# Optimization experiments

Measured on AMD Instinct MI355X. Metric: run time of the kernel, lower is better.

## Reference

```python
import jax, jax.numpy as jnp
import numpy as np

NEG = -1e32
EPS_LN = 1e-5

def _layer_norm(x, w, b):
    mu = jnp.mean(x, axis=-1, keepdims=True)
    var = jnp.mean((x - mu) ** 2, axis=-1, keepdims=True)
    return (x - mu) / jnp.sqrt(var + EPS_LN) * w + b

def setup_inputs() -> dict:
    key = jax.random.key(0)
    ks = jax.random.split(key, 10)
    B, S, D, H, F = 2, 2048, 1024, 16, 4096
    s = 0.02
    return {
        "query": jax.random.normal(ks[0], (B, S, D), jnp.float32),
        "key": jax.random.normal(ks[1], (B, S, D), jnp.float32),
        "values": jax.random.normal(ks[2], (B, S, D), jnp.float32),
        "Wk": jax.random.normal(ks[3], (D, D), jnp.float32) * s,
        "bk": jnp.zeros((D,), jnp.float32),
        "Wv": jax.random.normal(ks[4], (D, D), jnp.float32) * s,
        "bv": jnp.zeros((D,), jnp.float32),
        "Wo": jax.random.normal(ks[5], (D, D), jnp.float32) * s,
        "bo": jnp.zeros((D,), jnp.float32),
        "gammas": jax.random.normal(ks[6], (H, 1, 1), jnp.float32),
        "ln1_w": jnp.ones((D,), jnp.float32),
        "ln1_b": jnp.zeros((D,), jnp.float32),
        "W1": jax.random.normal(ks[7], (F, D), jnp.float32) * s,
        "b1": jnp.zeros((F,), jnp.float32),
        "W2": jax.random.normal(ks[8], (D, F), jnp.float32) * s,
        "b2": jnp.zeros((D,), jnp.float32),
        "ln2_w": jnp.ones((D,), jnp.float32),
        "ln2_b": jnp.zeros((D,), jnp.float32),
        "mask": 1,
    }

def _forward(query, key, values, Wk, bk, Wv, bv, Wo, bo, gammas,
             ln1_w, ln1_b, W1, b1, W2, b2, ln2_w, ln2_b, mask):
    B, S, D = query.shape
    H = gammas.shape[0]
    dk = D // H
    # kq_same=True: q and k both use k_linear
    def proj(x, W, b):
        return (x @ W.T + b).reshape(B, S, H, dk).transpose(0, 2, 1, 3)  # bhsd
    q = proj(query, Wk, bk)
    k = proj(key, Wk, bk)
    v = proj(values, Wv, bv)

    scores = jnp.einsum("bhqd,bhkd->bhqk", q, k) / np.sqrt(dk).astype(np.float32)
    # src_mask: np.triu(ones, k=mask)==0 -> allowed where j <= i + mask - 1
    allow = jnp.tril(jnp.ones((S, S), bool), k=mask - 1)[None, None]  # (1,1,S,S)

    # --- distance decay (no_grad block in torch) ---
    scores_ = jax.nn.softmax(jnp.where(allow, scores, NEG), axis=-1)
    scores_ = scores_ * allow.astype(scores_.dtype)
    distcum = jnp.cumsum(scores_, axis=-1)
    disttotal = jnp.sum(scores_, axis=-1, keepdims=True)
    idx = jnp.arange(S)
    position_effect = jnp.abs(idx[:, None] - idx[None, :]).astype(jnp.float32)[None, None]
    dist_scores = jnp.sqrt(jnp.clip((disttotal - distcum) * position_effect, 0.0, None))
    gamma = -jax.nn.softplus(gammas)[None]  # (1,H,1,1)
    total_effect = jnp.clip(jnp.exp(dist_scores * gamma), 1e-5, 1e5)
    total_effect = jax.lax.stop_gradient(total_effect)
    # ---

    scores = scores * total_effect
    scores = jnp.where(allow, scores, NEG)
    attn = jax.nn.softmax(scores, axis=-1)
    out = jnp.einsum("bhqk,bhkd->bhqd", attn, v)
    concat = out.transpose(0, 2, 1, 3).reshape(B, S, D)
    query2 = concat @ Wo.T + bo

    x = _layer_norm(query + query2, ln1_w, ln1_b)
    ff = jax.nn.relu(x @ W1.T + b1) @ W2.T + b2
    x = _layer_norm(x + ff, ln2_w, ln2_b)
    return x

def reference(query, key, values, Wk, bk, Wv, bv, Wo, bo, gammas,
              ln1_w, ln1_b, W1, b1, W2, b2, ln2_w, ln2_b, mask):
    return _forward(query, key, values, Wk, bk, Wv, bv, Wo, bo, gammas,
                    ln1_w, ln1_b, W1, b1, W2, b2, ln2_w, ln2_b, mask)
```

## Files before the change

kernel.cpp:

```cpp
#include <hip/hip_runtime.h>
#include <hip/hip_bf16.h>

#define B_   2
#define S_   2048
#define D_   1024
#define H_   16
#define DK_  64
#define F_   4096
#define M_   (B_*S_)
#define PD   72

typedef __attribute__((ext_vector_type(8))) short short8;
typedef __attribute__((ext_vector_type(4))) float f32x4;

__device__ __forceinline__ float bf2f(unsigned short s) { return __uint_as_float(((unsigned int)s) << 16); }
__device__ __forceinline__ unsigned short f2bf(float f) {
    unsigned int u = __float_as_uint(f);
    u += 0x7fffu + ((u >> 16) & 1u);
    return (unsigned short)(u >> 16);
}

__device__ __forceinline__ bool probe_f32(const unsigned int* p) {
    return *p == 0x3F800000u;
}
__device__ __forceinline__ float ld1e(const void* p, size_t idx, bool f32) {
    return f32 ? ((const float*)p)[idx] : bf2f(((const unsigned short*)p)[idx]);
}
__device__ __forceinline__ void st1e(void* p, size_t idx, bool f32, float v) {
    if (f32) ((float*)p)[idx] = v;
    else     ((unsigned short*)p)[idx] = f2bf(v);
}

__device__ __forceinline__ void async16(void* lds, const void* g) {
    __builtin_amdgcn_global_load_lds(
        (const __attribute__((address_space(1))) void*)g,
        (__attribute__((address_space(3))) void*)lds, 16, 0, 0);
}

__device__ __forceinline__ unsigned int cvt_pk_bf16(float a, float b) {
    unsigned int r;
    asm("v_cvt_pk_bf16_f32 %0, %1, %2" : "=v"(r) : "v"(a), "v"(b));
    return r;
}

template <bool IS_MAX>
__device__ __forceinline__ float block_reduce(float val, float* buf, int tid) {
    buf[tid] = val;
    __syncthreads();
    #pragma unroll
    for (int off = 128; off > 0; off >>= 1) {
        if (tid < off) {
            float o = buf[tid + off];
            buf[tid] = IS_MAX ? fmaxf(buf[tid], o) : (buf[tid] + o);
        }
        __syncthreads();
    }
    float r = buf[0];
    __syncthreads();
    return r;
}

__global__ __launch_bounds__(256) void cvt_all(
    const void* __restrict__ W1, const void* __restrict__ W2,
    const void* __restrict__ Wk, const void* __restrict__ Wv,
    const void* __restrict__ Wo,
    const void* __restrict__ Qi, const void* __restrict__ Ki,
    const void* __restrict__ Vi,
    unsigned short* __restrict__ W1b, unsigned short* __restrict__ W2b,
    unsigned short* __restrict__ Wkb, unsigned short* __restrict__ Wvb,
    unsigned short* __restrict__ Wob,
    unsigned short* __restrict__ qcb, unsigned short* __restrict__ kcb,
    unsigned short* __restrict__ vcb,
    const unsigned int* __restrict__ probe)
{
    const bool p32 = probe_f32(probe);
    const int blk = blockIdx.x;
    const void* src;
    unsigned short* dst;
    int off;
    if (blk < 2048)      { src = W1; dst = W1b; off = blk; }
    else if (blk < 4096) { src = W2; dst = W2b; off = blk - 2048; }
    else if (blk < 4608) { src = Wk; dst = Wkb; off = blk - 4096; }
    else if (blk < 5120) { src = Wv; dst = Wvb; off = blk - 4608; }
    else if (blk < 5632) { src = Wo; dst = Wob; off = blk - 5120; }
    else if (blk < 7680) { if (!p32) return; src = Qi; dst = qcb; off = blk - 5632; }
    else if (blk < 9728) { if (!p32) return; src = Ki; dst = kcb; off = blk - 7680; }
    else                 { if (!p32) return; src = Vi; dst = vcb; off = blk - 9728; }
    const int i8 = (off * 256 + threadIdx.x) * 8;
    if (p32) {
        const float4 a = *(const float4*)((const float*)src + i8);
        const float4 b = *(const float4*)((const float*)src + i8 + 4);
        short8 o;
        o[0] = (short)f2bf(a.x); o[1] = (short)f2bf(a.y);
        o[2] = (short)f2bf(a.z); o[3] = (short)f2bf(a.w);
        o[4] = (short)f2bf(b.x); o[5] = (short)f2bf(b.y);
        o[6] = (short)f2bf(b.z); o[7] = (short)f2bf(b.w);
        *(short8*)(dst + i8) = o;
    } else {
        *(uint4*)(dst + i8) = *(const uint4*)((const unsigned short*)src + i8);
    }
}

template <int RELU, int AEXT, int CEXT>
__device__ __forceinline__ void gemm_body(
    const void* __restrict__ A,
    const unsigned short* __restrict__ W,
    const void* __restrict__ bias,
    void* __restrict__ C,
    int M, int N, int K, bool p32, int bx, int by)
{
    __shared__ unsigned short As[2][128 * 32];
    __shared__ unsigned short Ws[2][128 * 32];

    const bool a32 = AEXT && p32;
    const bool c32 = CEXT && p32;

    const int tid = threadIdx.x;
    const int lane = tid & 63;
    const int w = tid >> 6;
    const int wr = w >> 1;
    const int wc = w & 1;
    const int col16 = lane & 15;
    const int quad = lane >> 4;

    const int m0 = by * 128;
    const int n0 = bx * 128;

    const int c0 = tid, c1 = 256 + tid;
    const int r0 = c0 >> 2, kc0 = (((c0 & 3) ^ ((c0 >> 3) & 3)) * 8);
    const int r1 = c1 >> 2, kc1 = (((c1 & 3) ^ ((c1 >> 3) & 3)) * 8);

    const int fcol = ((quad ^ ((col16 >> 1) & 3)) * 8);

    f32x4 acc[4][4];
    #pragma unroll
    for (int mt = 0; mt < 4; mt++)
        #pragma unroll
        for (int nt = 0; nt < 4; nt++)
            acc[mt][nt] = (f32x4){0.f, 0.f, 0.f, 0.f};

    auto stage = [&](int bb, int k0) {
        async16(&Ws[bb][c0 * 8], W + (size_t)(n0 + r0) * K + k0 + kc0);
        async16(&Ws[bb][c1 * 8], W + (size_t)(n0 + r1) * K + k0 + kc1);
        if (a32) {
            const float* a0 = (const float*)A + (size_t)(m0 + r0) * K + k0 + kc0;
            const float* a1 = (const float*)A + (size_t)(m0 + r1) * K + k0 + kc1;
            const float4 x0 = *(const float4*)a0, y0 = *(const float4*)(a0 + 4);
            const float4 x1 = *(const float4*)a1, y1 = *(const float4*)(a1 + 4);
            short8 s0, s1;
            s0[0] = (short)f2bf(x0.x); s0[1] = (short)f2bf(x0.y);
            s0[2] = (short)f2bf(x0.z); s0[3] = (short)f2bf(x0.w);
            s0[4] = (short)f2bf(y0.x); s0[5] = (short)f2bf(y0.y);
            s0[6] = (short)f2bf(y0.z); s0[7] = (short)f2bf(y0.w);
            s1[0] = (short)f2bf(x1.x); s1[1] = (short)f2bf(x1.y);
            s1[2] = (short)f2bf(x1.z); s1[3] = (short)f2bf(x1.w);
            s1[4] = (short)f2bf(y1.x); s1[5] = (short)f2bf(y1.y);
            s1[6] = (short)f2bf(y1.z); s1[7] = (short)f2bf(y1.w);
            *(short8*)&As[bb][c0 * 8] = s0;
            *(short8*)&As[bb][c1 * 8] = s1;
        } else {
            const unsigned short* Ab = (const unsigned short*)A;
            async16(&As[bb][c0 * 8], Ab + (size_t)(m0 + r0) * K + k0 + kc0);
            async16(&As[bb][c1 * 8], Ab + (size_t)(m0 + r1) * K + k0 + kc1);
        }
    };

    stage(0, 0);
    __syncthreads();
    int cur = 0;
    for (int k0 = 0; k0 < K; k0 += 32) {
        const int nxt = cur ^ 1;
        if (k0 + 32 < K) stage(nxt, k0 + 32);

        short8 av[4], bv[4];
        #pragma unroll
        for (int mt = 0; mt < 4; mt++)
            av[mt] = *(const short8*)&As[cur][(wr * 64 + mt * 16 + col16) * 32 + fcol];
        #pragma unroll
        for (int nt = 0; nt < 4; nt++)
            bv[nt] = *(const short8*)&Ws[cur][(wc * 64 + nt * 16 + col16) * 32 + fcol];
        #pragma unroll
        for (int mt = 0; mt < 4; mt++)
            #pragma unroll
            for (int nt = 0; nt < 4; nt++)
                acc[mt][nt] = __builtin_amdgcn_mfma_f32_16x16x32_bf16(
                    av[mt], bv[nt], acc[mt][nt], 0, 0, 0);
        __syncthreads();
        cur = nxt;
    }

    #pragma unroll
    for (int mt = 0; mt < 4; mt++) {
        const int row = m0 + wr * 64 + mt * 16 + quad * 4;
        #pragma unroll
        for (int nt = 0; nt < 4; nt++) {
            const int col = n0 + wc * 64 + nt * 16 + col16;
            const float bb = ld1e(bias, col, p32);
            #pragma unroll
            for (int r = 0; r < 4; r++) {
                float v = acc[mt][nt][r] + bb;
                if (RELU) v = fmaxf(v, 0.f);
                st1e(C, (size_t)(row + r) * N + col, c32, v);
            }
        }
    }
}

template <int RELU, int AEXT, int CEXT>
__global__ __launch_bounds__(256) void gemm_mf(
    const void* __restrict__ A,
    const unsigned short* __restrict__ W,
    const void* __restrict__ bias,
    void* __restrict__ C,
    int M, int N, int K,
    const unsigned int* __restrict__ probe)
{
    gemm_body<RELU, AEXT, CEXT>(A, W, bias, C, M, N, K, probe_f32(probe),
                                blockIdx.x, blockIdx.y);
}

template <int RELU, int CEXT>
__global__ __launch_bounds__(1024) void gemm_sk(
    const unsigned short* __restrict__ A,
    const unsigned short* __restrict__ W,
    const void* __restrict__ bias,
    void* __restrict__ C,
    int M, int N, int K,
    const unsigned int* __restrict__ probe)
{
    __shared__ unsigned short SS[4][2][2][128 * 32];
    float* const R0 = (float*)&SS[0][0][0][0];
    float* const R1 = (float*)&SS[2][0][0][0];

    const bool p32 = probe_f32(probe);
    const bool c32 = CEXT && p32;

    const int tid = threadIdx.x;
    const int g = tid >> 8;
    const int tl = tid & 255;
    const int lane = tl & 63;
    const int w = tl >> 6;
    const int wr = w >> 1;
    const int wc = w & 1;
    const int col16 = lane & 15;
    const int quad = lane >> 4;

    const int m0 = blockIdx.y * 128;
    const int n0 = blockIdx.x * 128;

    const int c0 = tl, c1 = 256 + tl;
    const int r0 = c0 >> 2, kc0 = (((c0 & 3) ^ ((c0 >> 3) & 3)) * 8);
    const int r1 = c1 >> 2, kc1 = (((c1 & 3) ^ ((c1 >> 3) & 3)) * 8);
    const int fcol = ((quad ^ ((col16 >> 1) & 3)) * 8);

    const int Kq = K >> 2;
    const int kbeg = g * Kq;

    f32x4 acc[4][4];
    #pragma unroll
    for (int mt = 0; mt < 4; mt++)
        #pragma unroll
        for (int nt = 0; nt < 4; nt++)
            acc[mt][nt] = (f32x4){0.f, 0.f, 0.f, 0.f};

    auto stage = [&](int bb, int k0) {
        async16(&SS[g][bb][1][c0 * 8], W + (size_t)(n0 + r0) * K + k0 + kc0);
        async16(&SS[g][bb][1][c1 * 8], W + (size_t)(n0 + r1) * K + k0 + kc1);
        async16(&SS[g][bb][0][c0 * 8], A + (size_t)(m0 + r0) * K + k0 + kc0);
        async16(&SS[g][bb][0][c1 * 8], A + (size_t)(m0 + r1) * K + k0 + kc1);
    };

    stage(0, kbeg);
    __syncthreads();
    int cur = 0;
    for (int kk = 0; kk < Kq; kk += 32) {
        const int nxt = cur ^ 1;
        if (kk + 32 < Kq) stage(nxt, kbeg + kk + 32);

        short8 av[4], bv[4];
        #pragma unroll
        for (int mt = 0; mt < 4; mt++)
            av[mt] = *(const short8*)&SS[g][cur][0][(wr * 64 + mt * 16 + col16) * 32 + fcol];
        #pragma unroll
        for (int nt = 0; nt < 4; nt++)
            bv[nt] = *(const short8*)&SS[g][cur][1][(wc * 64 + nt * 16 + col16) * 32 + fcol];
        #pragma unroll
        for (int mt = 0; mt < 4; mt++)
            #pragma unroll
            for (int nt = 0; nt < 4; nt++)
                acc[mt][nt] = __builtin_amdgcn_mfma_f32_16x16x32_bf16(
                    av[mt], bv[nt], acc[mt][nt], 0, 0, 0);
        __syncthreads();
        cur = nxt;
    }

    if (g == 1 || g == 3) {
        float* R = (g == 1) ? R0 : R1;
        #pragma unroll
        for (int mt = 0; mt < 4; mt++)
            #pragma unroll
            for (int nt = 0; nt < 4; nt++) {
                const int lrow = wr * 64 + mt * 16 + quad * 4;
                const int lcol = wc * 64 + nt * 16 + col16;
                #pragma unroll
                for (int r = 0; r < 4; r++)
                    R[(lrow + r) * 128 + lcol] = acc[mt][nt][r];
            }
    }
    __syncthreads();
    if (g == 0 || g == 2) {
        const float* R = (g == 0) ? R0 : R1;
        #pragma unroll
        for (int mt = 0; mt < 4; mt++)
            #pragma unroll
            for (int nt = 0; nt < 4; nt++) {
                const int lrow = wr * 64 + mt * 16 + quad * 4;
                const int lcol = wc * 64 + nt * 16 + col16;
                #pragma unroll
                for (int r = 0; r < 4; r++)
                    acc[mt][nt][r] += R[(lrow + r) * 128 + lcol];
            }
    }
    __syncthreads();
    if (g == 2) {
        #pragma unroll
        for (int mt = 0; mt < 4; mt++)
            #pragma unroll
            for (int nt = 0; nt < 4; nt++) {
                const int lrow = wr * 64 + mt * 16 + quad * 4;
                const int lcol = wc * 64 + nt * 16 + col16;
                #pragma unroll
                for (int r = 0; r < 4; r++)
                    R0[(lrow + r) * 128 + lcol] = acc[mt][nt][r];
            }
    }
    __syncthreads();
    if (g == 0) {
        #pragma unroll
        for (int mt = 0; mt < 4; mt++) {
            const int lrow = wr * 64 + mt * 16 + quad * 4;
            const int row = m0 + lrow;
            #pragma unroll
            for (int nt = 0; nt < 4; nt++) {
                const int lcol = wc * 64 + nt * 16 + col16;
                const int col = n0 + lcol;
                const float bb = ld1e(bias, col, p32);
                #pragma unroll
                for (int r = 0; r < 4; r++) {
                    float v = acc[mt][nt][r] + R0[(lrow + r) * 128 + lcol] + bb;
                    if (RELU) v = fmaxf(v, 0.f);
                    st1e(C, (size_t)(row + r) * N + col, c32, v);
                }
            }
        }
    }
}

__global__ __launch_bounds__(256) void gemm_proj(
    const void* __restrict__ q_orig, const void* __restrict__ k_orig,
    const void* __restrict__ v_orig,
    const unsigned short* __restrict__ qcb, const unsigned short* __restrict__ kcb,
    const unsigned short* __restrict__ vcb,
    const unsigned short* __restrict__ Wkb, const unsigned short* __restrict__ Wvb,
    const void* __restrict__ bk, const void* __restrict__ bv,
    unsigned short* __restrict__ qw, unsigned short* __restrict__ kw,
    unsigned short* __restrict__ vw,
    const unsigned int* __restrict__ probe)
{
    const bool p32 = probe_f32(probe);
    const int z = blockIdx.z;
    const unsigned short* W = (z == 2) ? Wvb : Wkb;
    const void* bias = (z == 2) ? bv : bk;
    void* C = (z == 0) ? (void*)qw : (z == 1) ? (void*)kw : (void*)vw;
    if (z == 2 && p32 && vcb == nullptr) {
        gemm_body<0, 1, 0>(v_orig, W, bias, C, M_, D_, D_, p32,
                           blockIdx.x, blockIdx.y);
    } else {
        const void* A = (z == 0) ? (p32 ? (const void*)qcb : q_orig)
                      : (z == 1) ? (p32 ? (const void*)kcb : k_orig)
                                 : (p32 ? (const void*)vcb : v_orig);
        gemm_body<0, 0, 0>(A, W, bias, C, M_, D_, D_, p32,
                           blockIdx.x, blockIdx.y);
    }
}

__global__ __launch_bounds__(256) void vtrans(
    const unsigned short* __restrict__ vw,
    unsigned short* __restrict__ vtg)
{
    __shared__ unsigned short T[64 * PD];
    const int tid = threadIdx.x;
    const int bid = blockIdx.x;
    const int bh = bid & 31;
    const int kt = bid >> 5;
    const int h = bh & 15, b = bh >> 4;
    #pragma unroll
    for (int cc = 0; cc < 2; cc++) {
        const int c = tid + cc * 256;
        const int key = c >> 3, dc = c & 7;
        const uint4 u = *(const uint4*)(vw + (size_t)(b * S_ + kt * 64 + key) * D_ + h * 64 + dc * 8);
        unsigned short* dst = &T[(dc * 8) * PD + key];
        dst[0 * PD] = (unsigned short)(u.x & 0xffff);
        dst[1 * PD] = (unsigned short)(u.x >> 16);
        dst[2 * PD] = (unsigned short)(u.y & 0xffff);
        dst[3 * PD] = (unsigned short)(u.y >> 16);
        dst[4 * PD] = (unsigned short)(u.z & 0xffff);
        dst[5 * PD] = (unsigned short)(u.z >> 16);
        dst[6 * PD] = (unsigned short)(u.w & 0xffff);
        dst[7 * PD] = (unsigned short)(u.w >> 16);
    }
    __syncthreads();
    #pragma unroll
    for (int cc = 0; cc < 2; cc++) {
        const int c = tid + cc * 256;
        const int d = c >> 3, kc = c & 7;
        const uint4 u = *(const uint4*)&T[d * PD + kc * 8];
        *(uint4*)(vtg + ((size_t)bh * 64 + d) * S_ + kt * 64 + kc * 8) = u;
    }
}

__global__ __launch_bounds__(256) void attn_mfma(
    const unsigned short* __restrict__ qw,
    const unsigned short* __restrict__ kw,
    const unsigned short* __restrict__ vtg,
    const void* __restrict__ gam,
    const int* __restrict__ maskp,
    unsigned short* __restrict__ outc,
    const unsigned int* __restrict__ probe)
{
    __shared__ unsigned short Qs[64 * PD];
    __shared__ unsigned short Ks[64 * PD];
    __shared__ unsigned short Vt[64 * PD];
    unsigned int* const Pu = (unsigned int*)Qs;

    const bool p32 = probe_f32(probe);
    const int tid = threadIdx.x;
    const int lane = tid & 63;
    const int w = tid >> 6;
    const int col16 = lane & 15;
    const int quad = lane >> 4;
    const int bid = blockIdx.x;
    const int qt = 31 - (bid >> 5);
    const int bh = bid & 31;
    const int h = bh & 15;
    const int b = bh >> 4;
    const int i0 = qt * 64;

    const int mask = *maskp;
    long long nje = (long long)i0 + 63 + (long long)mask;
    int njmax = (nje > S_) ? S_ : (int)nje;
    if (njmax < 1) njmax = 1;
    const int ntiles = (njmax + 63) >> 6;
    long long fm = (long long)i0 + (long long)mask - 64;
    int nfull = 0;
    if (fm >= 0) {
        long long v = (fm >> 6) + 1;
        nfull = (v > ntiles) ? ntiles : (int)v;
    }

    const float L2E = 1.44269504088896f;
    const float gval = ld1e(gam, h, p32);
    const float sp = (gval > 20.f) ? gval : log1pf(__expf(gval));
    const float g2 = -sp * L2E;
    const float SC2 = 0.125f * L2E;

    const int myrow = i0 + w * 16 + col16;
    const int limq = myrow + mask - quad * 4;

    #pragma unroll
    for (int cc = 0; cc < 2; cc++) {
        const int c = tid + cc * 256;
        const int row = c >> 3, dc = c & 7;
        const uint4 u = *(const uint4*)(qw + (size_t)(b * S_ + i0 + row) * D_ + h * 64 + dc * 8);
        *(uint4*)&Qs[row * PD + dc * 8] = u;
    }
    __syncthreads();

    short8 avq[2];
    #pragma unroll
    for (int ks = 0; ks < 2; ks++)
        avq[ks] = *(const short8*)&Qs[(w * 16 + col16) * PD + ks * 32 + quad * 8];

    float T1l = 0.f;
    for (int t = 0; t < ntiles; t++) {
        const int j0 = t * 64;
        __syncthreads();
        #pragma unroll
        for (int cc = 0; cc < 2; cc++) {
            const int c = tid + cc * 256;
            const int row = c >> 3, dc = c & 7;
            const uint4 u = *(const uint4*)(kw + (size_t)(b * S_ + j0 + row) * D_ + h * 64 + dc * 8);
            *(uint4*)&Ks[row * PD + dc * 8] = u;
        }
        __syncthreads();

        f32x4 acc[4];
        #pragma unroll
        for (int nt = 0; nt < 4; nt++) acc[nt] = (f32x4){0.f, 0.f, 0.f, 0.f};
        #pragma unroll
        for (int ks = 0; ks < 2; ks++)
            #pragma unroll
            for (int nt = 0; nt < 4; nt++) {
                const short8 kv = *(const short8*)&Ks[(nt * 16 + col16) * PD + ks * 32 + quad * 8];
                acc[nt] = __builtin_amdgcn_mfma_f32_16x16x32_bf16(kv, avq[ks], acc[nt], 0, 0, 0);
            }

        if (t >= nfull) {
            #pragma unroll
            for (int nt = 0; nt < 4; nt++) {
                const int Ln = limq - j0 - nt * 16;
                #pragma unroll
                for (int r = 0; r < 4; r++)
                    acc[nt][r] = (r < Ln) ? acc[nt][r] : -3.0e38f;
            }
        }

        #pragma unroll
        for (int nt = 0; nt < 4; nt++)
            #pragma unroll
            for (int r = 0; r < 4; r++)
                T1l += __builtin_amdgcn_exp2f(acc[nt][r] * SC2);
    }
    T1l += __shfl_xor(T1l, 16, 64);
    T1l += __shfl_xor(T1l, 32, 64);
    const float rT1 = 1.0f / T1l;

    float l2 = 0.f;
    float Cb_run = 0.f;
    f32x4 O[4];
    #pragma unroll
    for (int nt = 0; nt < 4; nt++) O[nt] = (f32x4){0.f, 0.f, 0.f, 0.f};

    for (int t = 0; t < ntiles; t++) {
        const int j0 = t * 64;
        __syncthreads();
        #pragma unroll
        for (int cc = 0; cc < 2; cc++) {
            const int c = tid + cc * 256;
            const int row = c >> 3, dc = c & 7;
            const uint4 u = *(const uint4*)(kw + (size_t)(b * S_ + j0 + row) * D_ + h * 64 + dc * 8);
            *(uint4*)&Ks[row * PD + dc * 8] = u;
        }
        #pragma unroll
        for (int cc = 0; cc < 2; cc++) {
            const int c = tid + cc * 256;
            const int d = c >> 3, kc = c & 7;
            const uint4 u = *(const uint4*)(vtg + ((size_t)bh * 64 + d) * S_ + j0 + kc * 8);
            *(uint4*)&Vt[d * PD + kc * 8] = u;
        }
        __syncthreads();

        f32x4 acc[4];
        #pragma unroll
        for (int nt = 0; nt < 4; nt++) acc[nt] = (f32x4){0.f, 0.f, 0.f, 0.f};
        #pragma unroll
        for (int ks = 0; ks < 2; ks++)
            #pragma unroll
            for (int nt = 0; nt < 4; nt++) {
                const short8 kv = *(const short8*)&Ks[(nt * 16 + col16) * PD + ks * 32 + quad * 8];
                acc[nt] = __builtin_amdgcn_mfma_f32_16x16x32_bf16(kv, avq[ks], acc[nt], 0, 0, 0);
            }

        if (t >= nfull) {
            #pragma unroll
            for (int nt = 0; nt < 4; nt++) {
                const int Ln = limq - j0 - nt * 16;
                #pragma unroll
                for (int r = 0; r < 4; r++)
                    acc[nt][r] = (r < Ln) ? acc[nt][r] : -3.0e38f;
            }
        }

        float s2v[4][4], loc[4][4], run4[4];
        #pragma unroll
        for (int nt = 0; nt < 4; nt++) {
            float rr = 0.f;
            #pragma unroll
            for (int r = 0; r < 4; r++) {
                const float s2 = acc[nt][r] * SC2;
                s2v[nt][r] = s2;
                rr += __builtin_amdgcn_exp2f(s2);
                loc[nt][r] = rr;
            }
            run4[nt] = rr;
        }
        float excl[4], tot[4];
        #pragma unroll
        for (int nt = 0; nt < 4; nt++) {
            float v = run4[nt];
            const float u1 = __shfl_up(v, 16, 64); if (quad >= 1) v += u1;
            const float u2 = __shfl_up(v, 32, 64); if (quad >= 2) v += u2;
            excl[nt] = v - run4[nt];
            tot[nt] = __shfl(v, col16 + 48, 64);
        }

        float Cb = Cb_run;
        #pragma unroll
        for (int nt = 0; nt < 4; nt++) {
            const float CeR = (Cb + excl[nt]) * rT1;
            const float d0f = (float)(myrow - j0 - nt * 16 - quad * 4);
            float p4[4];
            #pragma unroll
            for (int r = 0; r < 4; r++) {
                const float cumn = __builtin_fmaf(loc[nt][r], rT1, CeR);
                const float rem = fmaxf(1.f - cumn, 0.f);
                const float pe = fabsf(d0f - (float)r);
                const float te = fmaxf(
                    __builtin_amdgcn_exp2f(g2 * __builtin_amdgcn_sqrtf(rem * pe)), 1e-5f);
                const float tv = s2v[nt][r] * te;
                p4[r] = __builtin_amdgcn_exp2f(tv);
                l2 += p4[r];
            }
            uint2 pk;
            pk.x = cvt_pk_bf16(p4[0], p4[1]);
            pk.y = cvt_pk_bf16(p4[2], p4[3]);
            *(uint2*)&Pu[(w * 16 + col16) * 36 + nt * 8 + quad * 2] = pk;
            Cb += tot[nt];
        }
        Cb_run = Cb;

        const short8 pa0 = *(const short8*)&Pu[(w * 16 + col16) * 36 + 0 * 16 + quad * 4];
        const short8 pa1 = *(const short8*)&Pu[(w * 16 + col16) * 36 + 1 * 16 + quad * 4];
        #pragma unroll
        for (int nt = 0; nt < 4; nt++) {
            const short8 bv0 = *(const short8*)&Vt[(nt * 16 + col16) * PD + 0 * 32 + quad * 8];
            const short8 bv1 = *(const short8*)&Vt[(nt * 16 + col16) * PD + 1 * 32 + quad * 8];
            O[nt] = __builtin_amdgcn_mfma_f32_16x16x32_bf16(pa0, bv0, O[nt], 0, 0, 0);
            O[nt] = __builtin_amdgcn_mfma_f32_16x16x32_bf16(pa1, bv1, O[nt], 0, 0, 0);
        }
    }

    l2 += __shfl_xor(l2, 16, 64);
    l2 += __shfl_xor(l2, 32, 64);
    const float rl2 = 1.0f / l2;
    float rl2O[4];
    #pragma unroll
    for (int r = 0; r < 4; r++) rl2O[r] = __shfl(rl2, quad * 4 + r, 64);
    #pragma unroll
    for (int nt = 0; nt < 4; nt++)
        #pragma unroll
        for (int r = 0; r < 4; r++)
            outc[(size_t)(b * S_ + i0 + w * 16 + quad * 4 + r) * D_ + h * 64 + nt * 16 + col16] =
                f2bf(O[nt][r] * rl2O[r]);
}

__global__ __launch_bounds__(256) void ln_fused(
    const void* __restrict__ A,
    const void* __restrict__ Bq,
    const void* __restrict__ w,
    const void* __restrict__ bias,
    void* __restrict__ out,
    const unsigned int* __restrict__ probe, int aext, int bext, int oext)
{
    __shared__ float xs[D_];
    __shared__ float red[256];
    const bool p32 = probe_f32(probe);
    const bool a32 = aext && p32;
    const bool b32 = bext && p32;
    const bool o32 = oext && p32;

    const int tid = threadIdx.x;
    const size_t row = (size_t)blockIdx.x * D_;

    float lsum = 0.f;
    #pragma unroll
    for (int qq = 0; qq < 4; qq++) {
        const int j = tid + qq * 256;
        const float x = ld1e(A, row + j, a32) + ld1e(Bq, row + j, b32);
        xs[j] = x;
        lsum += x;
    }
    const float mu = block_reduce<false>(lsum, red, tid) * (1.0f / D_);

    float lv = 0.f;
    #pragma unroll
    for (int qq = 0; qq < 4; qq++) {
        const int j = tid + qq * 256;
        const float dd = xs[j] - mu;
        lv += dd * dd;
    }
    const float var = block_reduce<false>(lv, red, tid) * (1.0f / D_);
    const float rs = rsqrtf(var + 1e-5f);

    #pragma unroll
    for (int qq = 0; qq < 4; qq++) {
        const int j = tid + qq * 256;
        const float o = (xs[j] - mu) * rs * ld1e(w, j, p32) + ld1e(bias, j, p32);
        st1e(out, row + j, o32, o);
    }
}

extern "C" void kernel_launch(void* const* d_in, const int* in_sizes, int n_in,
                              void* d_out, int out_size, void* d_ws, size_t ws_size,
                              hipStream_t stream)
{
    (void)in_sizes; (void)n_in; (void)out_size;

    const void* query  = d_in[0];
    const void* key_   = d_in[1];
    const void* values = d_in[2];
    const void* Wk     = d_in[3];
    const void* bk     = d_in[4];
    const void* Wv     = d_in[5];
    const void* bv     = d_in[6];
    const void* Wo     = d_in[7];
    const void* bo     = d_in[8];
    const void* gammas = d_in[9];
    const void* ln1w   = d_in[10];
    const void* ln1b   = d_in[11];
    const void* W1     = d_in[12];
    const void* b1     = d_in[13];
    const void* W2     = d_in[14];
    const void* b2     = d_in[15];
    const void* ln2w   = d_in[16];
    const void* ln2b   = d_in[17];
    const int*  maskp  = (const int*)d_in[18];
    const unsigned int* probe = (const unsigned int*)ln1w;

    char* ws = (char*)d_ws;
    const size_t MiB = 1024 * 1024;
    unsigned short* W1b = (unsigned short*)(ws + 0 * MiB);
    unsigned short* W2b = (unsigned short*)(ws + 8 * MiB);
    unsigned short* Wkb = (unsigned short*)(ws + 16 * MiB);
    unsigned short* Wvb = (unsigned short*)(ws + 18 * MiB);
    unsigned short* Wob = (unsigned short*)(ws + 20 * MiB);
    unsigned short* qw  = (unsigned short*)(ws + 22 * MiB);
    unsigned short* kw  = (unsigned short*)(ws + 30 * MiB);
    unsigned short* vw  = (unsigned short*)(ws + 38 * MiB);
    unsigned short* cw  = (unsigned short*)(ws + 46 * MiB);
    unsigned short* vtg = (unsigned short*)(ws + 54 * MiB);
    unsigned short* x1  = (unsigned short*)(ws + 22 * MiB);
    unsigned short* fh  = (unsigned short*)(ws + 30 * MiB);
    unsigned short* qc  = (unsigned short*)(ws + 46 * MiB);
    unsigned short* kc  = (unsigned short*)(ws + 54 * MiB);
    unsigned short* vc  = (ws_size >= (size_t)70 * MiB)
                          ? (unsigned short*)(ws + 62 * MiB) : nullptr;

    const dim3 blk(256);
    const dim3 blk10(1024);
    const int cvtgrid = vc ? 11776 : 9728;
    cvt_all<<<dim3(cvtgrid), blk, 0, stream>>>(
        W1, W2, Wk, Wv, Wo, query, key_, values,
        W1b, W2b, Wkb, Wvb, Wob, qc, kc, vc, probe);
    gemm_proj<<<dim3(D_ / 128, M_ / 128, 3), blk, 0, stream>>>(
        query, key_, values, qc, kc, vc, Wkb, Wvb, bk, bv, qw, kw, vw, probe);
    vtrans<<<dim3(1024), blk, 0, stream>>>(vw, vtg);
    attn_mfma<<<dim3(B_ * H_ * (S_ / 64)), blk, 0, stream>>>(
        qw, kw, vtg, gammas, maskp, cw, probe);
    gemm_sk<0, 0><<<dim3(D_ / 128, M_ / 128), blk10, 0, stream>>>(
        cw, Wob, bo, x1, M_, D_, D_, probe);
    ln_fused<<<dim3(M_), blk, 0, stream>>>(query, x1, ln1w, ln1b, x1, probe, 1, 0, 0);
    gemm_mf<1, 0, 0><<<dim3(F_ / 128, M_ / 128), blk, 0, stream>>>(
        x1, W1b, b1, fh, M_, F_, D_, probe);
    gemm_sk<0, 1><<<dim3(D_ / 128, M_ / 128), blk10, 0, stream>>>(
        fh, W2b, b2, d_out, M_, D_, F_, probe);
    ln_fused<<<dim3(M_), blk, 0, stream>>>(x1, d_out, ln2w, ln2b, d_out, probe, 0, 1, 1);
}
```

Measured before the change: 454.4 us.

## Fuse V transpose into projection GEMM, cache per-tile column sums, vectorize layernorm

The V projection GEMM now writes its output already transposed into the per-head layout through an LDS staging tile, so the separate vtrans kernel and its round trip through global memory are removed. In attention, the first pass stores per-tile row sums in shared memory and turns them into prefix sums, which replaces the running carry used in the second pass. The layernorm kernel loads and stores four contiguous elements per thread with vector accesses. These changes add LDS use in the GEMM and attention kernels, which may lower occupancy, and the ctS buffer assumes at most 33 key tiles.

```diff
diff --git a/kernel.cpp b/kernel.cpp
--- a/kernel.cpp
+++ b/kernel.cpp
@@ -101,7 +101,7 @@
     }
 }
 
-template <int RELU, int AEXT, int CEXT>
+template <int RELU, int AEXT, int CEXT, int VT>
 __device__ __forceinline__ void gemm_body(
     const void* __restrict__ A,
     const unsigned short* __restrict__ W,
@@ -111,6 +111,7 @@
 {
     __shared__ unsigned short As[2][128 * 32];
     __shared__ unsigned short Ws[2][128 * 32];
+    __shared__ __align__(16) unsigned short Tt[VT ? 64 * 136 : 1];
 
     const bool a32 = AEXT && p32;
     const bool c32 = CEXT && p32;
@@ -189,6 +190,40 @@
         cur = nxt;
     }
 
+    if constexpr (VT) {
+        unsigned short* vtg = (unsigned short*)C;
+        const int b = m0 >> 11;
+        const int s0 = m0 & (S_ - 1);
+        const int h0 = n0 >> 6;
+        #pragma unroll
+        for (int hh = 0; hh < 2; hh++) {
+            __syncthreads();
+            if (wc == hh) {
+                #pragma unroll
+                for (int mt = 0; mt < 4; mt++) {
+                    const int sloc = wr * 64 + mt * 16 + quad * 4;
+                    #pragma unroll
+                    for (int nt = 0; nt < 4; nt++) {
+                        const int dloc = nt * 16 + col16;
+                        const float bb = ld1e(bias, n0 + hh * 64 + dloc, p32);
+                        #pragma unroll
+                        for (int r = 0; r < 4; r++)
+                            Tt[dloc * 136 + sloc + r] = f2bf(acc[mt][nt][r] + bb);
+                    }
+                }
+            }
+            __syncthreads();
+            #pragma unroll
+            for (int cc = 0; cc < 4; cc++) {
+                const int idx = tid + cc * 256;
+                const int d = idx >> 4, sc = idx & 15;
+                const uint4 u = *(const uint4*)&Tt[d * 136 + sc * 8];
+                *(uint4*)(vtg + ((size_t)((b * 16 + h0 + hh) * 64 + d)) * S_ + s0 + sc * 8) = u;
+            }
+        }
+        return;
+    }
+
     #pragma unroll
     for (int mt = 0; mt < 4; mt++) {
         const int row = m0 + wr * 64 + mt * 16 + quad * 4;
@@ -215,8 +250,8 @@
     int M, int N, int K,
     const unsigned int* __restrict__ probe)
 {
-    gemm_body<RELU, AEXT, CEXT>(A, W, bias, C, M, N, K, probe_f32(probe),
-                                blockIdx.x, blockIdx.y);
+    gemm_body<RELU, AEXT, CEXT, 0>(A, W, bias, C, M, N, K, probe_f32(probe),
+                                   blockIdx.x, blockIdx.y);
 }
 
 template <int RELU, int CEXT>
@@ -364,58 +399,26 @@
     const unsigned short* __restrict__ Wkb, const unsigned short* __restrict__ Wvb,
     const void* __restrict__ bk, const void* __restrict__ bv,
     unsigned short* __restrict__ qw, unsigned short* __restrict__ kw,
-    unsigned short* __restrict__ vw,
+    unsigned short* __restrict__ vtg,
     const unsigned int* __restrict__ probe)
 {
     const bool p32 = probe_f32(probe);
     const int z = blockIdx.z;
-    const unsigned short* W = (z == 2) ? Wvb : Wkb;
-    const void* bias = (z == 2) ? bv : bk;
-    void* C = (z == 0) ? (void*)qw : (z == 1) ? (void*)kw : (void*)vw;
-    if (z == 2 && p32 && vcb == nullptr) {
-        gemm_body<0, 1, 0>(v_orig, W, bias, C, M_, D_, D_, p32,
-                           blockIdx.x, blockIdx.y);
+    if (z == 2) {
+        if (p32 && vcb == nullptr) {
+            gemm_body<0, 1, 0, 1>(v_orig, Wvb, bv, (void*)vtg, M_, D_, D_, p32,
+                                  blockIdx.x, blockIdx.y);
+        } else {
+            const void* A = p32 ? (const void*)vcb : v_orig;
+            gemm_body<0, 0, 0, 1>(A, Wvb, bv, (void*)vtg, M_, D_, D_, p32,
+                                  blockIdx.x, blockIdx.y);
+        }
     } else {
         const void* A = (z == 0) ? (p32 ? (const void*)qcb : q_orig)
-                      : (z == 1) ? (p32 ? (const void*)kcb : k_orig)
-                                 : (p32 ? (const void*)vcb : v_orig);
-        gemm_body<0, 0, 0>(A, W, bias, C, M_, D_, D_, p32,
-                           blockIdx.x, blockIdx.y);
-    }
-}
-
-__global__ __launch_bounds__(256) void vtrans(
-    const unsigned short* __restrict__ vw,
-    unsigned short* __restrict__ vtg)
-{
-    __shared__ unsigned short T[64 * PD];
-    const int tid = threadIdx.x;
-    const int bid = blockIdx.x;
-    const int bh = bid & 31;
-    const int kt = bid >> 5;
-    const int h = bh & 15, b = bh >> 4;
-    #pragma unroll
-    for (int cc = 0; cc < 2; cc++) {
-        const int c = tid + cc * 256;
-        const int key = c >> 3, dc = c & 7;
-        const uint4 u = *(const uint4*)(vw + (size_t)(b * S_ + kt * 64 + key) * D_ + h * 64 + dc * 8);
-        unsigned short* dst = &T[(dc * 8) * PD + key];
-        dst[0 * PD] = (unsigned short)(u.x & 0xffff);
-        dst[1 * PD] = (unsigned short)(u.x >> 16);
-        dst[2 * PD] = (unsigned short)(u.y & 0xffff);
-        dst[3 * PD] = (unsigned short)(u.y >> 16);
-        dst[4 * PD] = (unsigned short)(u.z & 0xffff);
-        dst[5 * PD] = (unsigned short)(u.z >> 16);
-        dst[6 * PD] = (unsigned short)(u.w & 0xffff);
-        dst[7 * PD] = (unsigned short)(u.w >> 16);
-    }
-    __syncthreads();
-    #pragma unroll
-    for (int cc = 0; cc < 2; cc++) {
-        const int c = tid + cc * 256;
-        const int d = c >> 3, kc = c & 7;
-        const uint4 u = *(const uint4*)&T[d * PD + kc * 8];
-        *(uint4*)(vtg + ((size_t)bh * 64 + d) * S_ + kt * 64 + kc * 8) = u;
+                                 : (p32 ? (const void*)kcb : k_orig);
+        void* C = (z == 0) ? (void*)qw : (void*)kw;
+        gemm_body<0, 0, 0, 0>(A, Wkb, bk, C, M_, D_, D_, p32,
+                              blockIdx.x, blockIdx.y);
     }
 }
 
@@ -431,6 +434,8 @@
     __shared__ unsigned short Qs[64 * PD];
     __shared__ unsigned short Ks[64 * PD];
     __shared__ unsigned short Vt[64 * PD];
+    __shared__ float ctS[64 * 33];
+    __shared__ float rT1S[64];
     unsigned int* const Pu = (unsigned int*)Qs;
 
     const bool p32 = probe_f32(probe);
@@ -481,7 +486,6 @@
     for (int ks = 0; ks < 2; ks++)
         avq[ks] = *(const short8*)&Qs[(w * 16 + col16) * PD + ks * 32 + quad * 8];
 
-    float T1l = 0.f;
     for (int t = 0; t < ntiles; t++) {
         const int j0 = t * 64;
         __syncthreads();
@@ -515,18 +519,35 @@
             }
         }
 
+        float cs = 0.f;
         #pragma unroll
         for (int nt = 0; nt < 4; nt++)
             #pragma unroll
             for (int r = 0; r < 4; r++)
-                T1l += __builtin_amdgcn_exp2f(acc[nt][r] * SC2);
-    }
-    T1l += __shfl_xor(T1l, 16, 64);
-    T1l += __shfl_xor(T1l, 32, 64);
-    const float rT1 = 1.0f / T1l;
+                cs += __builtin_amdgcn_exp2f(acc[nt][r] * SC2);
+        cs += __shfl_xor(cs, 16, 64);
+        cs += __shfl_xor(cs, 32, 64);
+
+        if (lane < 16)
+            ctS[(w * 16 + lane) * 33 + t] = cs;
+    }
+
+    __syncthreads();
+    if (lane < 16) {
+        const int row = w * 16 + lane;
+        float runv = 0.f;
+        for (int t = 0; t < ntiles; t++) {
+            const float e = ctS[row * 33 + t];
+            ctS[row * 33 + t] = runv;
+            runv += e;
+        }
+        rT1S[row] = 1.0f / runv;
+    }
+    __syncthreads();
+
+    const float rT1 = rT1S[w * 16 + col16];
 
     float l2 = 0.f;
-    float Cb_run = 0.f;
     f32x4 O[4];
     #pragma unroll
     for (int nt = 0; nt < 4; nt++) O[nt] = (f32x4){0.f, 0.f, 0.f, 0.f};
@@ -594,7 +615,8 @@
             tot[nt] = __shfl(v, col16 + 48, 64);
         }
 
-        float Cb = Cb_run;
+        const float pref = ctS[(w * 16 + col16) * 33 + t];
+        float Cb = pref;
         #pragma unroll
         for (int nt = 0; nt < 4; nt++) {
             const float CeR = (Cb + excl[nt]) * rT1;
@@ -617,7 +639,6 @@
             *(uint2*)&Pu[(w * 16 + col16) * 36 + nt * 8 + quad * 2] = pk;
             Cb += tot[nt];
         }
-        Cb_run = Cb;
 
         const short8 pa0 = *(const short8*)&Pu[(w * 16 + col16) * 36 + 0 * 16 + quad * 4];
         const short8 pa1 = *(const short8*)&Pu[(w * 16 + col16) * 36 + 1 * 16 + quad * 4];
@@ -661,32 +682,69 @@
 
     const int tid = threadIdx.x;
     const size_t row = (size_t)blockIdx.x * D_;
+    const int j4 = tid * 4;
+
+    float xa[4], xb[4];
+    if (a32) {
+        const float4 t = *(const float4*)((const float*)A + row + j4);
+        xa[0] = t.x; xa[1] = t.y; xa[2] = t.z; xa[3] = t.w;
+    } else {
+        const ushort4 t = *(const ushort4*)((const unsigned short*)A + row + j4);
+        xa[0] = bf2f(t.x); xa[1] = bf2f(t.y); xa[2] = bf2f(t.z); xa[3] = bf2f(t.w);
+    }
+    if (b32) {
+        const float4 t = *(const float4*)((const float*)Bq + row + j4);
+        xb[0] = t.x; xb[1] = t.y; xb[2] = t.z; xb[3] = t.w;
+    } else {
+        const ushort4 t = *(const ushort4*)((const unsigned short*)Bq + row + j4);
+        xb[0] = bf2f(t.x); xb[1] = bf2f(t.y); xb[2] = bf2f(t.z); xb[3] = bf2f(t.w);
+    }
 
     float lsum = 0.f;
-    #pragma unroll
-    for (int qq = 0; qq < 4; qq++) {
-        const int j = tid + qq * 256;
-        const float x = ld1e(A, row + j, a32) + ld1e(Bq, row + j, b32);
-        xs[j] = x;
-        lsum += x;
+    float x4[4];
+    #pragma unroll
+    for (int k = 0; k < 4; k++) {
+        x4[k] = xa[k] + xb[k];
+        xs[j4 + k] = x4[k];
+        lsum += x4[k];
     }
     const float mu = block_reduce<false>(lsum, red, tid) * (1.0f / D_);
 
     float lv = 0.f;
     #pragma unroll
-    for (int qq = 0; qq < 4; qq++) {
-        const int j = tid + qq * 256;
-        const float dd = xs[j] - mu;
+    for (int k = 0; k < 4; k++) {
+        const float dd = x4[k] - mu;
         lv += dd * dd;
     }
     const float var = block_reduce<false>(lv, red, tid) * (1.0f / D_);
     const float rs = rsqrtf(var + 1e-5f);
 
-    #pragma unroll
-    for (int qq = 0; qq < 4; qq++) {
-        const int j = tid + qq * 256;
-        const float o = (xs[j] - mu) * rs * ld1e(w, j, p32) + ld1e(bias, j, p32);
-        st1e(out, row + j, o32, o);
+    float wv[4], bv[4];
+    if (p32) {
+        const float4 tw = *(const float4*)((const float*)w + j4);
+        const float4 tb = *(const float4*)((const float*)bias + j4);
+        wv[0] = tw.x; wv[1] = tw.y; wv[2] = tw.z; wv[3] = tw.w;
+        bv[0] = tb.x; bv[1] = tb.y; bv[2] = tb.z; bv[3] = tb.w;
+    } else {
+        const ushort4 tw = *(const ushort4*)((const unsigned short*)w + j4);
+        const ushort4 tb = *(const ushort4*)((const unsigned short*)bias + j4);
+        wv[0] = bf2f(tw.x); wv[1] = bf2f(tw.y); wv[2] = bf2f(tw.z); wv[3] = bf2f(tw.w);
+        bv[0] = bf2f(tb.x); bv[1] = bf2f(tb.y); bv[2] = bf2f(tb.z); bv[3] = bf2f(tb.w);
+    }
+
+    float o4[4];
+    #pragma unroll
+    for (int k = 0; k < 4; k++)
+        o4[k] = (x4[k] - mu) * rs * wv[k] + bv[k];
+
+    if (o32) {
+        float4 o; o.x = o4[0]; o.y = o4[1]; o.z = o4[2]; o.w = o4[3];
+        *(float4*)((float*)out + row + j4) = o;
+    } else {
+        uint2 pk;
+        pk.x = cvt_pk_bf16(o4[0], o4[1]);
+        pk.y = cvt_pk_bf16(o4[2], o4[3]);
+        *(uint2*)((unsigned short*)out + row + j4) = pk;
     }
 }
 
@@ -726,9 +784,8 @@
     unsigned short* Wob = (unsigned short*)(ws + 20 * MiB);
     unsigned short* qw  = (unsigned short*)(ws + 22 * MiB);
     unsigned short* kw  = (unsigned short*)(ws + 30 * MiB);
-    unsigned short* vw  = (unsigned short*)(ws + 38 * MiB);
+    unsigned short* vtg = (unsigned short*)(ws + 38 * MiB);
     unsigned short* cw  = (unsigned short*)(ws + 46 * MiB);
-    unsigned short* vtg = (unsigned short*)(ws + 54 * MiB);
     unsigned short* x1  = (unsigned short*)(ws + 22 * MiB);
     unsigned short* fh  = (unsigned short*)(ws + 30 * MiB);
     unsigned short* qc  = (unsigned short*)(ws + 46 * MiB);
@@ -743,8 +800,7 @@
         W1, W2, Wk, Wv, Wo, query, key_, values,
         W1b, W2b, Wkb, Wvb, Wob, qc, kc, vc, probe);
     gemm_proj<<<dim3(D_ / 128, M_ / 128, 3), blk, 0, stream>>>(
-        query, key_, values, qc, kc, vc, Wkb, Wvb, bk, bv, qw, kw, vw, probe);
-    vtrans<<<dim3(1024), blk, 0, stream>>>(vw, vtg);
+        query, key_, values, qc, kc, vc, Wkb, Wvb, bk, bv, qw, kw, vtg, probe);
     attn_mfma<<<dim3(B_ * H_ * (S_ / 64)), blk, 0, stream>>>(
         qw, kw, vtg, gammas, maskp, cw, probe);
     gemm_sk<0, 0><<<dim3(D_ / 128, M_ / 128), blk10, 0, stream>>>(
```

Measured after the change: 457.3 us. Within noise of the previous version (+0.6%).
